# Optimization experiments

Hardware: AMD Instinct MI355X
Metric: run time of the kernel (lower is better)

The kernel has to match this reference:

```python
import jax, jax.numpy as jnp
import numpy as np

N = 32768
E = 524288
NFEAT = 256
NHID = 256
NUM_HEADS = 4
HEAD_DIM = NHID // NUM_HEADS
NLAYER = 2
EPS = 1e-5


def setup_inputs():
    keys = iter(jax.random.split(jax.random.key(0), 64))

    def nrm(shape, scale=0.05):
        return jax.random.normal(next(keys), shape, dtype=jnp.float32) * scale

    inp = {
        "x": jax.random.normal(next(keys), (N, NFEAT), dtype=jnp.float32),
        "edge_src": jax.random.randint(next(keys), (E,), 0, N),
        "edge_dst": jax.random.randint(next(keys), (E,), 0, N),
        "edge_attr": jax.random.uniform(next(keys), (E,), dtype=jnp.float32) * 0.1,
        "num_graphs": 64,
    }
    for i in range(NLAYER):
        fin = NFEAT if i == 0 else NHID
        inp["conv_w%d" % i] = nrm((fin, NHID))
        inp["bn_g%d" % i] = jnp.ones((NHID,), jnp.float32)
        inp["bn_b%d" % i] = jnp.zeros((NHID,), jnp.float32)
        inp["bn_m%d" % i] = nrm((NHID,), 0.1)
        inp["bn_v%d" % i] = 1.0 + jax.random.uniform(next(keys), (NHID,), dtype=jnp.float32) * 0.1
        inp["attn_in_w%d" % i] = nrm((3 * NHID, NHID))
        inp["attn_in_b%d" % i] = jnp.zeros((3 * NHID,), jnp.float32)
        inp["attn_out_w%d" % i] = nrm((NHID, NHID))
        inp["attn_out_b%d" % i] = jnp.zeros((NHID,), jnp.float32)
        inp["ln_g%d" % i] = jnp.ones((NHID,), jnp.float32)
        inp["ln_b%d" % i] = jnp.zeros((NHID,), jnp.float32)
    inp["score_w"] = nrm((1, NHID))
    inp["score_b"] = jnp.zeros((1,), jnp.float32)
    return inp


def _mha(xb, iw, ib, ow, ob):
    # torch.nn.MultiheadAttention (batch_first), all graphs same length so
    # key_padding_mask is all-False (no masked positions).
    B, S, H = xb.shape
    q, k, v = jnp.split(xb @ iw.T + ib, 3, axis=-1)
    heads = lambda t: t.reshape(B, S, NUM_HEADS, HEAD_DIM).transpose(0, 2, 1, 3)
    q, k, v = heads(q), heads(k), heads(v)
    scale = jnp.float32(1.0 / np.sqrt(HEAD_DIM))
    att = jax.nn.softmax(jnp.einsum("bhqd,bhkd->bhqk", q, k) * scale, axis=-1)
    o = jnp.einsum("bhqk,bhkd->bhqd", att, v).transpose(0, 2, 1, 3).reshape(B, S, H)
    return o @ ow.T + ob


def _forward(x, edge_attr, params, edge_src, edge_dst, num_graphs):
    n = x.shape[0]
    B = num_graphs
    S = n // B  # equal-sized graphs -> max_nodes == S, pad is a no-op
    h = x
    for i, (cw, bng, bnb, bnm, bnv, iw, ib, ow, ob, lg, lb) in enumerate(params):
        # DIGCNConv: out[dst] += edge_attr * (x @ W)[src]
        conv = jax.ops.segment_sum(edge_attr[:, None] * (h @ cw)[edge_src], edge_dst, num_segments=n)
        # BatchNorm1d (eval mode, running stats)
        conv = (conv - bnm) * jax.lax.rsqrt(bnv + EPS) * bng + bnb
        # ragged gather -> pad/stack -> MHA -> unpad (equal graph sizes => reshape)
        attended = _mha(conv.reshape(B, S, NHID), iw, ib, ow, ob).reshape(n, NHID)
        y = conv + attended
        mu = jnp.mean(y, axis=-1, keepdims=True)
        var = jnp.mean((y - mu) ** 2, axis=-1, keepdims=True)
        h = (y - mu) * jax.lax.rsqrt(var + EPS) * lg + lb  # LayerNorm
        if i < NLAYER - 1:
            h = jax.nn.relu(h)
    return h


def reference(x, edge_src, edge_dst, edge_attr, num_graphs,
              conv_w0, bn_g0, bn_b0, bn_m0, bn_v0, attn_in_w0, attn_in_b0, attn_out_w0, attn_out_b0, ln_g0, ln_b0,
              conv_w1, bn_g1, bn_b1, bn_m1, bn_v1, attn_in_w1, attn_in_b1, attn_out_w1, attn_out_b1, ln_g1, ln_b1,
              score_w, score_b):
    params = [
        (conv_w0, bn_g0, bn_b0, bn_m0, bn_v0, attn_in_w0, attn_in_b0, attn_out_w0, attn_out_b0, ln_g0, ln_b0),
        (conv_w1, bn_g1, bn_b1, bn_m1, bn_v1, attn_in_w1, attn_in_b1, attn_out_w1, attn_out_b1, ln_g1, ln_b1),
    ]
    h = _forward(x, edge_attr, params, edge_src, edge_dst, num_graphs)
    scores = (h @ score_w.T + score_b)[:, 0]
    # emb_list / score_list are per-graph views of these flat arrays
    return h, scores
```

## Files before the change

kernel.cpp:

```cpp
#include <hip/hip_runtime.h>
#include <hip/hip_bf16.h>
#include <math.h>

#define N_NODES 32768
#define E_EDGES 524288
#define NHID    256
#define HEAD_DIM 64
#define SEQ     512
#define EPS_LN  1e-5f
#define SM_SCALE 0.18033688011112042f

typedef __hip_bfloat16 bf16;
typedef __attribute__((ext_vector_type(8))) short short8;
typedef __attribute__((ext_vector_type(4))) float floatx4;
static const size_t NH = (size_t)N_NODES * NHID;

__device__ __forceinline__ void unpack2(unsigned int u, float& lo, float& hi) {
    union { float f; unsigned int i; } a, b;
    a.i = u << 16; b.i = u & 0xffff0000u;
    lo = a.f; hi = b.f;
}

__device__ __forceinline__ void* swzp(void* base, int row, int col) {
    return (char*)base + (((row << 7) + (col << 1)) ^ ((row & 7) << 4));
}

__device__ __forceinline__ void gload16(const bf16* g, void* lds) {
    __builtin_amdgcn_global_load_lds((const __attribute__((address_space(1))) void*)g,
                                     (__attribute__((address_space(3))) void*)lds, 16, 0, 0);
}

__global__ void k_cvtb4(bf16* __restrict__ dst, const float* __restrict__ src) {
    size_t i = (size_t)(blockIdx.x * 256 + threadIdx.x) * 4;
    const float4 v = *(const float4*)(src + i);
    __align__(8) bf16 tmp[4];
    tmp[0] = __float2bfloat16(v.x);
    tmp[1] = __float2bfloat16(v.y);
    tmp[2] = __float2bfloat16(v.z);
    tmp[3] = __float2bfloat16(v.w);
    *(uint2*)(dst + i) = *(uint2*)tmp;
}

__global__ __launch_bounds__(256) void k_stage(const float* __restrict__ cw,
                                               const float* __restrict__ bng,
                                               const float* __restrict__ bnb,
                                               const float* __restrict__ bnm,
                                               const float* __restrict__ bnv,
                                               const float* __restrict__ iw,
                                               const float* __restrict__ ow,
                                               bf16* __restrict__ iwb,
                                               bf16* __restrict__ owb,
                                               bf16* __restrict__ cwT,
                                               float* __restrict__ bns,
                                               float* __restrict__ bnt) {
    const int blk = blockIdx.x;
    const int tid = threadIdx.x;
    if (blk < 256) {
        const float* src = (blk < 192) ? iw : ow;
        bf16* dst = (blk < 192) ? iwb : owb;
        size_t i = (size_t)((blk < 192 ? blk : blk - 192) * 256 + tid) * 4;
        const float4 v = *(const float4*)(src + i);
        __align__(8) bf16 t4[4];
        t4[0] = __float2bfloat16(v.x);
        t4[1] = __float2bfloat16(v.y);
        t4[2] = __float2bfloat16(v.z);
        t4[3] = __float2bfloat16(v.w);
        *(uint2*)(dst + i) = *(uint2*)t4;
    } else if (blk < 512) {
        const int k = blk - 256;
        cwT[(size_t)tid * 256 + k] = __float2bfloat16(cw[(size_t)k * 256 + tid]);
    } else {
        float sv = bng[tid] * rsqrtf(bnv[tid] + EPS_LN);
        bns[tid] = sv;
        bnt[tid] = bnb[tid] - bnm[tid] * sv;
    }
}

__global__ void k_hist(const int* __restrict__ edst, int* __restrict__ counts) {
    int e = blockIdx.x * 256 + threadIdx.x;
    atomicAdd(&counts[edst[e]], 1);
}

__global__ __launch_bounds__(256) void k_scan(const int* __restrict__ counts,
                                              int* __restrict__ offsets,
                                              int* __restrict__ cursor) {
    __shared__ int sums[256];
    const int tid = threadIdx.x;
    const int base = tid * 128;
    int s = 0;
    for (int i = 0; i < 128; ++i) s += counts[base + i];
    sums[tid] = s;
    __syncthreads();
    for (int off = 1; off < 256; off <<= 1) {
        int v = (tid >= off) ? sums[tid - off] : 0;
        __syncthreads();
        sums[tid] += v;
        __syncthreads();
    }
    int run = (tid == 0) ? 0 : sums[tid - 1];
    for (int i = 0; i < 128; ++i) {
        int c = counts[base + i];
        offsets[base + i] = run;
        cursor[base + i] = run;
        run += c;
    }
    if (tid == 255) offsets[32768] = run;
}

__global__ void k_fill(const int* __restrict__ esrc, const int* __restrict__ edst,
                       const float* __restrict__ eattr, int* __restrict__ cursor,
                       int* __restrict__ srcp, float* __restrict__ attrp) {
    int e = blockIdx.x * 256 + threadIdx.x;
    int d = edst[e];
    int slot = atomicAdd(&cursor[d], 1);
    srcp[slot] = esrc[e];
    attrp[slot] = eattr[e];
}

__global__ __launch_bounds__(256) void k_gather(const bf16* __restrict__ t,
                                                const int* __restrict__ offsets,
                                                const int* __restrict__ srcp,
                                                const float* __restrict__ attrp,
                                                const float* __restrict__ bns,
                                                const float* __restrict__ bnt,
                                                bf16* __restrict__ conv) {
    const int node = (blockIdx.x * 256 + threadIdx.x) >> 6;
    const int lane = threadIdx.x & 63;
    const int half = lane >> 5;
    const int l32 = lane & 31;
    const int start = offsets[node];
    const int end = offsets[node + 1];
    float a[8];
#pragma unroll
    for (int i = 0; i < 8; ++i) a[i] = 0.f;
    for (int c0 = start; c0 < end; c0 += 64) {
        const int n = min(64, end - c0);
        int sidx = 0;
        float sa = 0.f;
        if (lane < n) {
            sidx = srcp[c0 + lane];
            sa = attrp[c0 + lane];
        }
        for (int j = 0; j < n; j += 2) {
            const int e = j + half;
            const int s = __shfl(sidx, e, 64);
            const float aw = __shfl(sa, e, 64);
            const uint4 u = *(const uint4*)(t + (size_t)s * 256 + l32 * 8);
            float v0, v1, v2, v3, v4, v5, v6, v7;
            unpack2(u.x, v0, v1);
            unpack2(u.y, v2, v3);
            unpack2(u.z, v4, v5);
            unpack2(u.w, v6, v7);
            a[0] = fmaf(aw, v0, a[0]);
            a[1] = fmaf(aw, v1, a[1]);
            a[2] = fmaf(aw, v2, a[2]);
            a[3] = fmaf(aw, v3, a[3]);
            a[4] = fmaf(aw, v4, a[4]);
            a[5] = fmaf(aw, v5, a[5]);
            a[6] = fmaf(aw, v6, a[6]);
            a[7] = fmaf(aw, v7, a[7]);
        }
    }
#pragma unroll
    for (int i = 0; i < 8; ++i) a[i] += __shfl_xor(a[i], 32, 64);
    if (half == 0) {
        const int c = l32 * 8;
        const float4 s0 = *(const float4*)(bns + c);
        const float4 s1 = *(const float4*)(bns + c + 4);
        const float4 t0 = *(const float4*)(bnt + c);
        const float4 t1 = *(const float4*)(bnt + c + 4);
        __align__(16) bf16 tmp[8];
        tmp[0] = __float2bfloat16(fmaf(a[0], s0.x, t0.x));
        tmp[1] = __float2bfloat16(fmaf(a[1], s0.y, t0.y));
        tmp[2] = __float2bfloat16(fmaf(a[2], s0.z, t0.z));
        tmp[3] = __float2bfloat16(fmaf(a[3], s0.w, t0.w));
        tmp[4] = __float2bfloat16(fmaf(a[4], s1.x, t1.x));
        tmp[5] = __float2bfloat16(fmaf(a[5], s1.y, t1.y));
        tmp[6] = __float2bfloat16(fmaf(a[6], s1.z, t1.z));
        tmp[7] = __float2bfloat16(fmaf(a[7], s1.w, t1.w));
        *(uint4*)(conv + (size_t)node * 256 + c) = *(uint4*)tmp;
    }
}

__global__ __launch_bounds__(256) void k_gemm(const bf16* __restrict__ A,
                                              const bf16* __restrict__ WT,
                                              const float* __restrict__ bias,
                                              bf16* __restrict__ C, bf16* __restrict__ VT,
                                              int ldc, int qkvmode) {
    __shared__ __align__(16) short As[2][128 * 64];
    __shared__ __align__(16) short Bs[2][128 * 64];
    const int tid = threadIdx.x;
    const int bm = blockIdx.x * 128;
    const int bn = blockIdx.y * 128;
    const int wid = tid >> 6;
    const int lane = tid & 63;
    const int wr = (wid >> 1) * 64;
    const int wc = (wid & 1) * 64;
    const int quad = lane >> 4;
    const int l16 = lane & 15;

    floatx4 acc[4][4];
#pragma unroll
    for (int mi = 0; mi < 4; ++mi)
#pragma unroll
        for (int ni = 0; ni < 4; ++ni)
            acc[mi][ni] = (floatx4){0.f, 0.f, 0.f, 0.f};

    auto STAGE = [&](int ks, int bf) {
#pragma unroll
        for (int t = 0; t < 4; ++t) {
            const int p = ((t * 4 + wid) << 10) + (lane << 4);
            const int row = p >> 7;
            const int cb = (p & 127) ^ ((row & 7) << 4);
            gload16(A + (size_t)(bm + row) * 256 + ks * 64 + (cb >> 1),
                    (char*)&As[bf][0] + ((t * 4 + wid) << 10));
            gload16(WT + (size_t)(bn + row) * 256 + ks * 64 + (cb >> 1),
                    (char*)&Bs[bf][0] + ((t * 4 + wid) << 10));
        }
    };

    STAGE(0, 0);
    __syncthreads();
    for (int t = 0; t < 4; ++t) {
        const int buf = t & 1;
        if (t < 3) STAGE(t + 1, buf ^ 1);
#pragma unroll
        for (int kk = 0; kk < 2; ++kk) {
            const int kcol = kk * 32 + quad * 8;
            short8 af[4], bfr[4];
#pragma unroll
            for (int mi = 0; mi < 4; ++mi)
                af[mi] = *(const short8*)swzp(&As[buf][0], wr + mi * 16 + l16, kcol);
#pragma unroll
            for (int ni = 0; ni < 4; ++ni)
                bfr[ni] = *(const short8*)swzp(&Bs[buf][0], wc + ni * 16 + l16, kcol);
#pragma unroll
            for (int mi = 0; mi < 4; ++mi)
#pragma unroll
                for (int ni = 0; ni < 4; ++ni)
                    acc[mi][ni] = __builtin_amdgcn_mfma_f32_16x16x32_bf16(af[mi], bfr[ni],
                                                                          acc[mi][ni], 0, 0, 0);
        }
        __syncthreads();
    }
    const float cs = (qkvmode && bn < 256) ? SM_SCALE : 1.0f;
    const bool vpath = (qkvmode && bn >= 512);
#pragma unroll
    for (int ni = 0; ni < 4; ++ni) {
        const int gc = bn + wc + ni * 16 + l16;
        const float bv = bias ? bias[gc] : 0.f;
#pragma unroll
        for (int mi = 0; mi < 4; ++mi) {
            const int gr = bm + wr + mi * 16 + quad * 4;
            if (vpath) {
                const int head = (gc - 512) >> 6;
                const int d = (gc - 512) & 63;
                const int bg = gr >> 9;
                const int sl = gr & 511;
                __align__(8) bf16 t4[4];
#pragma unroll
                for (int r = 0; r < 4; ++r) t4[r] = __float2bfloat16(acc[mi][ni][r] + bv);
                *(uint2*)(VT + (((size_t)((bg * 4 + head) * 64 + d)) << 9) + sl) = *(uint2*)t4;
            } else {
#pragma unroll
                for (int r = 0; r < 4; ++r)
                    C[(size_t)(gr + r) * ldc + gc] = __float2bfloat16((acc[mi][ni][r] + bv) * cs);
            }
        }
    }
}

__global__ __launch_bounds__(256) void k_fattn(const bf16* __restrict__ qkv,
                                               const bf16* __restrict__ vtb,
                                               bf16* __restrict__ ctx) {
    const int bid = ((blockIdx.x & 7) << 8) | (blockIdx.x >> 3);
    const int qt = bid & 7;
    const int head = (bid >> 3) & 3;
    const int b = bid >> 5;
    const int tid = threadIdx.x;
    const int wave = tid >> 6;
    const int lane = tid & 63;
    const int quad = lane >> 4;
    const int l16 = lane & 15;
    const int qrow0 = b * SEQ + qt * 64 + wave * 16;

    __shared__ __align__(16) short Ks[2][64 * 64];
    __shared__ __align__(16) short Vt[2][64 * 64];
    __shared__ __align__(16) short Ps[4][16 * 64];

    const bf16* kbase = qkv + (size_t)(b * SEQ) * 768 + 256 + head * HEAD_DIM;
    const bf16* vbase = vtb + (size_t)((b * 4 + head) * 64) * 512;
    const int pbase = (wave << 10) + (lane << 4);

    short8 af_q[2];
    {
        const bf16* qp = qkv + (size_t)(qrow0 + l16) * 768 + head * HEAD_DIM + quad * 8;
        af_q[0] = *(const short8*)(qp);
        af_q[1] = *(const short8*)(qp + 32);
    }
    short8 ones;
#pragma unroll
    for (int j = 0; j < 8; ++j) ones[j] = (short)0x3F80;

    floatx4 acc[5];
#pragma unroll
    for (int nt = 0; nt < 5; ++nt) acc[nt] = (floatx4){0.f, 0.f, 0.f, 0.f};

    auto STAGE = [&](int kt2, int bf) {
#pragma unroll
        for (int i = 0; i < 2; ++i) {
            const int p = (i << 12) + pbase;
            const int row = p >> 7;
            const int cb = (p & 127) ^ ((row & 7) << 4);
            gload16(kbase + (size_t)(kt2 * 64 + row) * 768 + (cb >> 1),
                    (char*)Ks[bf] + (i << 12) + (wave << 10));
            gload16(vbase + (size_t)row * 512 + kt2 * 64 + (cb >> 1),
                    (char*)Vt[bf] + (i << 12) + (wave << 10));
        }
    };

    STAGE(0, 0);
    __syncthreads();

    for (int kt = 0; kt < 8; ++kt) {
        const int buf = kt & 1;
        if (kt < 7) STAGE(kt + 1, buf ^ 1);

        floatx4 sf[4];
#pragma unroll
        for (int f = 0; f < 4; ++f) {
            const short8 bk0 = *(const short8*)swzp(Ks[buf], f * 16 + l16, quad * 8);
            const short8 bk1 = *(const short8*)swzp(Ks[buf], f * 16 + l16, 32 + quad * 8);
            sf[f] = __builtin_amdgcn_mfma_f32_16x16x32_bf16(af_q[0], bk0,
                                                            (floatx4){0.f, 0.f, 0.f, 0.f}, 0, 0, 0);
            sf[f] = __builtin_amdgcn_mfma_f32_16x16x32_bf16(af_q[1], bk1, sf[f], 0, 0, 0);
        }

        bf16* psb = (bf16*)&Ps[wave][0];
#pragma unroll
        for (int r = 0; r < 4; ++r) {
            const float p0 = exp2f(fminf(sf[0][r], 80.f));
            const float p1 = exp2f(fminf(sf[1][r], 80.f));
            const float p2 = exp2f(fminf(sf[2][r], 80.f));
            const float p3 = exp2f(fminf(sf[3][r], 80.f));
            const int qr = quad * 4 + r;
            *(bf16*)swzp(psb, qr, l16)      = __float2bfloat16(p0);
            *(bf16*)swzp(psb, qr, 16 + l16) = __float2bfloat16(p1);
            *(bf16*)swzp(psb, qr, 32 + l16) = __float2bfloat16(p2);
            *(bf16*)swzp(psb, qr, 48 + l16) = __float2bfloat16(p3);
        }

#pragma unroll
        for (int c2 = 0; c2 < 2; ++c2) {
            const short8 ap = *(const short8*)swzp(psb, l16, c2 * 32 + quad * 8);
#pragma unroll
            for (int nt = 0; nt < 4; ++nt) {
                const short8 bv = *(const short8*)swzp(Vt[buf], nt * 16 + l16, c2 * 32 + quad * 8);
                acc[nt] = __builtin_amdgcn_mfma_f32_16x16x32_bf16(ap, bv, acc[nt], 0, 0, 0);
            }
            acc[4] = __builtin_amdgcn_mfma_f32_16x16x32_bf16(ap, ones, acc[4], 0, 0, 0);
        }
        __syncthreads();
    }

#pragma unroll
    for (int r = 0; r < 4; ++r) {
        const float inv = 1.f / acc[4][r];
        bf16* op = ctx + (size_t)(qrow0 + quad * 4 + r) * 256 + head * HEAD_DIM + l16;
        op[0]  = __float2bfloat16(acc[0][r] * inv);
        op[16] = __float2bfloat16(acc[1][r] * inv);
        op[32] = __float2bfloat16(acc[2][r] * inv);
        op[48] = __float2bfloat16(acc[3][r] * inv);
    }
}

__global__ void k_ln(const bf16* __restrict__ conv, const bf16* __restrict__ proj,
                     const float* __restrict__ lg, const float* __restrict__ lb,
                     bf16* __restrict__ h) {
    int gt = blockIdx.x * blockDim.x + threadIdx.x;
    int node = gt >> 6;
    int lane = gt & 63;
    size_t base = (size_t)node * 256 + lane * 4;
    uint2 ua = *(const uint2*)(conv + base);
    uint2 up = *(const uint2*)(proj + base);
    float a0, a1, a2, a3, p0, p1, p2, p3;
    unpack2(ua.x, a0, a1);
    unpack2(ua.y, a2, a3);
    unpack2(up.x, p0, p1);
    unpack2(up.y, p2, p3);
    float y0 = a0 + p0, y1 = a1 + p1, y2 = a2 + p2, y3 = a3 + p3;
    float sum = y0 + y1 + y2 + y3;
#pragma unroll
    for (int off = 32; off > 0; off >>= 1) sum += __shfl_xor(sum, off, 64);
    float mu = sum * (1.0f / 256.0f);
    float d0 = y0 - mu, d1 = y1 - mu, d2 = y2 - mu, d3 = y3 - mu;
    float vs = d0 * d0 + d1 * d1 + d2 * d2 + d3 * d3;
#pragma unroll
    for (int off = 32; off > 0; off >>= 1) vs += __shfl_xor(vs, off, 64);
    float r = rsqrtf(vs * (1.0f / 256.0f) + EPS_LN);
    int c = lane * 4;
    float o0 = fmaxf(fmaf(d0 * r, lg[c + 0], lb[c + 0]), 0.f);
    float o1 = fmaxf(fmaf(d1 * r, lg[c + 1], lb[c + 1]), 0.f);
    float o2 = fmaxf(fmaf(d2 * r, lg[c + 2], lb[c + 2]), 0.f);
    float o3 = fmaxf(fmaf(d3 * r, lg[c + 3], lb[c + 3]), 0.f);
    __align__(8) bf16 tmp[4];
    tmp[0] = __float2bfloat16(o0);
    tmp[1] = __float2bfloat16(o1);
    tmp[2] = __float2bfloat16(o2);
    tmp[3] = __float2bfloat16(o3);
    *(uint2*)(h + base) = *(uint2*)tmp;
}

__global__ void k_lnout(const bf16* __restrict__ conv, const bf16* __restrict__ proj,
                        const float* __restrict__ lg, const float* __restrict__ lb,
                        const float* __restrict__ sw, const float* __restrict__ sb,
                        float* __restrict__ out) {
    int gt = blockIdx.x * blockDim.x + threadIdx.x;
    int node = gt >> 6;
    int lane = gt & 63;
    size_t base = (size_t)node * 256 + lane * 4;
    uint2 ua = *(const uint2*)(conv + base);
    uint2 up = *(const uint2*)(proj + base);
    float a0, a1, a2, a3, p0, p1, p2, p3;
    unpack2(ua.x, a0, a1);
    unpack2(ua.y, a2, a3);
    unpack2(up.x, p0, p1);
    unpack2(up.y, p2, p3);
    float y0 = a0 + p0, y1 = a1 + p1, y2 = a2 + p2, y3 = a3 + p3;
    float sum = y0 + y1 + y2 + y3;
#pragma unroll
    for (int off = 32; off > 0; off >>= 1) sum += __shfl_xor(sum, off, 64);
    float mu = sum * (1.0f / 256.0f);
    float d0 = y0 - mu, d1 = y1 - mu, d2 = y2 - mu, d3 = y3 - mu;
    float vs = d0 * d0 + d1 * d1 + d2 * d2 + d3 * d3;
#pragma unroll
    for (int off = 32; off > 0; off >>= 1) vs += __shfl_xor(vs, off, 64);
    float r = rsqrtf(vs * (1.0f / 256.0f) + EPS_LN);
    int c = lane * 4;
    float o0 = fmaf(d0 * r, lg[c + 0], lb[c + 0]);
    float o1 = fmaf(d1 * r, lg[c + 1], lb[c + 1]);
    float o2 = fmaf(d2 * r, lg[c + 2], lb[c + 2]);
    float o3 = fmaf(d3 * r, lg[c + 3], lb[c + 3]);
    *(float4*)(out + base) = make_float4(o0, o1, o2, o3);
    float part = o0 * sw[c + 0] + o1 * sw[c + 1] + o2 * sw[c + 2] + o3 * sw[c + 3];
#pragma unroll
    for (int off = 32; off > 0; off >>= 1) part += __shfl_xor(part, off, 64);
    if (lane == 0)
        out[(size_t)N_NODES * 256 + node] = part + sb[0];
}

extern "C" void kernel_launch(void* const* d_in, const int* in_sizes, int n_in,
                              void* d_out, int out_size, void* d_ws, size_t ws_size,
                              hipStream_t stream) {
    if (ws_size < (size_t)100663296) return;

    const float* x     = (const float*)d_in[0];
    const int*   esrc  = (const int*)d_in[1];
    const int*   edst  = (const int*)d_in[2];
    const float* eattr = (const float*)d_in[3];

    bf16* convb = (bf16*)d_ws;
    bf16* qkvb  = convb + NH;
    bf16* tb    = qkvb + 3 * NH;
    bf16* vtb   = tb + NH;
    bf16* xb  = qkvb;
    bf16* hb  = qkvb + NH;
    bf16* pjb = qkvb;

    char* scr = (char*)d_out;
    const size_t LBYTES = 393216 + 131072 + 131072 + 2048;
    int*   counts  = (int*)(scr + 2 * LBYTES);
    int*   offsets = counts + 32768;
    int*   cursor  = offsets + 32769;
    int*   srcp    = cursor + 32768;
    float* attrp   = (float*)(srcp + E_EDGES);

    (void)hipMemsetAsync(counts, 0, 32768 * sizeof(int), stream);
    k_hist<<<E_EDGES / 256, 256, 0, stream>>>(edst, counts);
    k_scan<<<1, 256, 0, stream>>>(counts, offsets, cursor);
    k_fill<<<E_EDGES / 256, 256, 0, stream>>>(esrc, edst, eattr, cursor, srcp, attrp);

    for (int L = 0; L < 2; ++L) {
        int bi = 5 + L * 11;
        char* base = scr + (size_t)L * LBYTES;
        bf16*  iwb = (bf16*)base;
        bf16*  owb = iwb + 196608;
        bf16*  cwT = owb + 65536;
        float* bns = (float*)(cwT + 65536);
        float* bnt = bns + 256;
        k_stage<<<513, 256, 0, stream>>>((const float*)d_in[bi + 0], (const float*)d_in[bi + 1],
                                         (const float*)d_in[bi + 2], (const float*)d_in[bi + 3],
                                         (const float*)d_in[bi + 4], (const float*)d_in[bi + 5],
                                         (const float*)d_in[bi + 7], iwb, owb, cwT, bns, bnt);
    }

    k_cvtb4<<<8192, 256, 0, stream>>>(xb, x);

    for (int L = 0; L < 2; ++L) {
        int bi = 5 + L * 11;
        char* base = scr + (size_t)L * LBYTES;
        bf16*  iwb = (bf16*)base;
        bf16*  owb = iwb + 196608;
        bf16*  cwT = owb + 65536;
        float* bns = (float*)(cwT + 65536);
        float* bnt = bns + 256;
        const float* ib = (const float*)d_in[bi + 6];
        const float* ob = (const float*)d_in[bi + 8];

        k_gemm<<<dim3(256, 2), 256, 0, stream>>>(L == 0 ? xb : hb, cwT, nullptr, tb, nullptr,
                                                 256, 0);
        k_gather<<<8192, 256, 0, stream>>>(tb, offsets, srcp, attrp, bns, bnt, convb);
        k_gemm<<<dim3(256, 6), 256, 0, stream>>>(convb, iwb, ib, qkvb, vtb, 768, 1);
        k_fattn<<<2048, 256, 0, stream>>>(qkvb, vtb, tb);
        k_gemm<<<dim3(256, 2), 256, 0, stream>>>(tb, owb, ob, pjb, nullptr, 256, 0);
        if (L == 0) {
            k_ln<<<8192, 256, 0, stream>>>(convb, pjb, (const float*)d_in[bi + 9],
                                           (const float*)d_in[bi + 10], hb);
        } else {
            k_lnout<<<8192, 256, 0, stream>>>(convb, pjb, (const float*)d_in[bi + 9],
                                              (const float*)d_in[bi + 10],
                                              (const float*)d_in[27], (const float*)d_in[28],
                                              (float*)d_out);
        }
    }
}
```

Measured before the change: 507.5 us.

## Fuse out-proj GEMM with LayerNorm/score, merge staging launches, prefetch gather rows

```diff
diff --git a/kernel.cpp b/kernel.cpp
--- a/kernel.cpp
+++ b/kernel.cpp
@@ -30,35 +30,49 @@
                                      (__attribute__((address_space(3))) void*)lds, 16, 0, 0);
 }
 
-__global__ void k_cvtb4(bf16* __restrict__ dst, const float* __restrict__ src) {
-    size_t i = (size_t)(blockIdx.x * 256 + threadIdx.x) * 4;
-    const float4 v = *(const float4*)(src + i);
-    __align__(8) bf16 tmp[4];
-    tmp[0] = __float2bfloat16(v.x);
-    tmp[1] = __float2bfloat16(v.y);
-    tmp[2] = __float2bfloat16(v.z);
-    tmp[3] = __float2bfloat16(v.w);
-    *(uint2*)(dst + i) = *(uint2*)tmp;
-}
-
-__global__ __launch_bounds__(256) void k_stage(const float* __restrict__ cw,
-                                               const float* __restrict__ bng,
-                                               const float* __restrict__ bnb,
-                                               const float* __restrict__ bnm,
-                                               const float* __restrict__ bnv,
-                                               const float* __restrict__ iw,
-                                               const float* __restrict__ ow,
-                                               bf16* __restrict__ iwb,
-                                               bf16* __restrict__ owb,
-                                               bf16* __restrict__ cwT,
-                                               float* __restrict__ bns,
-                                               float* __restrict__ bnt) {
+__global__ __launch_bounds__(256) void k_stage2(
+    const float* __restrict__ cw0, const float* __restrict__ g0, const float* __restrict__ b0,
+    const float* __restrict__ m0, const float* __restrict__ v0, const float* __restrict__ iw0,
+    const float* __restrict__ ow0,
+    const float* __restrict__ cw1, const float* __restrict__ g1, const float* __restrict__ b1,
+    const float* __restrict__ m1, const float* __restrict__ v1, const float* __restrict__ iw1,
+    const float* __restrict__ ow1,
+    bf16* __restrict__ iwb0, bf16* __restrict__ owb0, bf16* __restrict__ cwT0,
+    float* __restrict__ bns0, float* __restrict__ bnt0,
+    bf16* __restrict__ iwb1, bf16* __restrict__ owb1, bf16* __restrict__ cwT1,
+    float* __restrict__ bns1, float* __restrict__ bnt1,
+    const float* __restrict__ x, bf16* __restrict__ xb) {
     const int blk = blockIdx.x;
     const int tid = threadIdx.x;
-    if (blk < 256) {
-        const float* src = (blk < 192) ? iw : ow;
-        bf16* dst = (blk < 192) ? iwb : owb;
-        size_t i = (size_t)((blk < 192 ? blk : blk - 192) * 256 + tid) * 4;
+    if (blk >= 1026) {
+        size_t i = (size_t)((blk - 1026) * 256 + tid) * 4;
+        const float4 v = *(const float4*)(x + i);
+        __align__(8) bf16 t4[4];
+        t4[0] = __float2bfloat16(v.x);
+        t4[1] = __float2bfloat16(v.y);
+        t4[2] = __float2bfloat16(v.z);
+        t4[3] = __float2bfloat16(v.w);
+        *(uint2*)(xb + i) = *(uint2*)t4;
+        return;
+    }
+    const int L = (blk >= 513);
+    const int b2 = L ? blk - 513 : blk;
+    const float* cw = L ? cw1 : cw0;
+    const float* bng = L ? g1 : g0;
+    const float* bnb = L ? b1 : b0;
+    const float* bnm = L ? m1 : m0;
+    const float* bnv = L ? v1 : v0;
+    const float* iw = L ? iw1 : iw0;
+    const float* ow = L ? ow1 : ow0;
+    bf16* iwb = L ? iwb1 : iwb0;
+    bf16* owb = L ? owb1 : owb0;
+    bf16* cwT = L ? cwT1 : cwT0;
+    float* bns = L ? bns1 : bns0;
+    float* bnt = L ? bnt1 : bnt0;
+    if (b2 < 256) {
+        const float* src = (b2 < 192) ? iw : ow;
+        bf16* dst = (b2 < 192) ? iwb : owb;
+        size_t i = (size_t)((b2 < 192 ? b2 : b2 - 192) * 256 + tid) * 4;
         const float4 v = *(const float4*)(src + i);
         __align__(8) bf16 t4[4];
         t4[0] = __float2bfloat16(v.x);
@@ -66,8 +80,8 @@
         t4[2] = __float2bfloat16(v.z);
         t4[3] = __float2bfloat16(v.w);
         *(uint2*)(dst + i) = *(uint2*)t4;
-    } else if (blk < 512) {
-        const int k = blk - 256;
+    } else if (b2 < 512) {
+        const int k = b2 - 256;
         cwT[(size_t)tid * 256 + k] = __float2bfloat16(cw[(size_t)k * 256 + tid]);
     } else {
         float sv = bng[tid] * rsqrtf(bnv[tid] + EPS_LN);
@@ -141,11 +155,14 @@
             sidx = srcp[c0 + lane];
             sa = attrp[c0 + lane];
         }
+        int s = __shfl(sidx, half, 64);
+        float aw = __shfl(sa, half, 64);
+        uint4 u = *(const uint4*)(t + (size_t)s * 256 + l32 * 8);
         for (int j = 0; j < n; j += 2) {
-            const int e = j + half;
-            const int s = __shfl(sidx, e, 64);
-            const float aw = __shfl(sa, e, 64);
-            const uint4 u = *(const uint4*)(t + (size_t)s * 256 + l32 * 8);
+            const int e2 = (j + 2 + half) & 63;
+            const int s2 = __shfl(sidx, e2, 64);
+            const float aw2 = __shfl(sa, e2, 64);
+            const uint4 u2 = *(const uint4*)(t + (size_t)s2 * 256 + l32 * 8);
             float v0, v1, v2, v3, v4, v5, v6, v7;
             unpack2(u.x, v0, v1);
             unpack2(u.y, v2, v3);
@@ -159,6 +176,8 @@
             a[5] = fmaf(aw, v5, a[5]);
             a[6] = fmaf(aw, v6, a[6]);
             a[7] = fmaf(aw, v7, a[7]);
+            u = u2;
+            aw = aw2;
         }
     }
 #pragma unroll
@@ -270,6 +289,194 @@
     }
 }
 
+__global__ __launch_bounds__(256) void k_gemmln(const bf16* __restrict__ A,
+                                                const bf16* __restrict__ WT,
+                                                const float* __restrict__ bias,
+                                                const bf16* __restrict__ conv,
+                                                const float* __restrict__ lg,
+                                                const float* __restrict__ lb,
+                                                bf16* __restrict__ h,
+                                                const float* __restrict__ sw,
+                                                const float* __restrict__ sb,
+                                                float* __restrict__ out, int mode) {
+    __shared__ __align__(16) short As[2][64 * 64];
+    __shared__ __align__(16) short Bs[2][256 * 64];
+    const int tid = threadIdx.x;
+    const int bm = blockIdx.x * 64;
+    const int wid = tid >> 6;
+    const int lane = tid & 63;
+    const int wc = wid * 64;
+    const int quad = lane >> 4;
+    const int l16 = lane & 15;
+
+    floatx4 acc[4][4];
+#pragma unroll
+    for (int mi = 0; mi < 4; ++mi)
+#pragma unroll
+        for (int ni = 0; ni < 4; ++ni)
+            acc[mi][ni] = (floatx4){0.f, 0.f, 0.f, 0.f};
+
+    auto STAGE = [&](int ks, int bf) {
+#pragma unroll
+        for (int t = 0; t < 2; ++t) {
+            const int base = (t * 4 + wid) << 10;
+            const int p = base + (lane << 4);
+            const int row = p >> 7;
+            const int cb = (p & 127) ^ ((row & 7) << 4);
+            gload16(A + (size_t)(bm + row) * 256 + ks * 64 + (cb >> 1),
+                    (char*)&As[bf][0] + base);
+        }
+#pragma unroll
+        for (int t = 0; t < 8; ++t) {
+            const int base = (t * 4 + wid) << 10;
+            const int p = base + (lane << 4);
+            const int row = p >> 7;
+            const int cb = (p & 127) ^ ((row & 7) << 4);
+            gload16(WT + (size_t)row * 256 + ks * 64 + (cb >> 1), (char*)&Bs[bf][0] + base);
+        }
+    };
+
+    STAGE(0, 0);
+    __syncthreads();
+    for (int t = 0; t < 4; ++t) {
+        const int buf = t & 1;
+        if (t < 3) STAGE(t + 1, buf ^ 1);
+#pragma unroll
+        for (int kk = 0; kk < 2; ++kk) {
+            const int kcol = kk * 32 + quad * 8;
+            short8 af[4], bfr[4];
+#pragma unroll
+            for (int mi = 0; mi < 4; ++mi)
+                af[mi] = *(const short8*)swzp(&As[buf][0], mi * 16 + l16, kcol);
+#pragma unroll
+            for (int ni = 0; ni < 4; ++ni)
+                bfr[ni] = *(const short8*)swzp(&Bs[buf][0], wc + ni * 16 + l16, kcol);
+#pragma unroll
+            for (int mi = 0; mi < 4; ++mi)
+#pragma unroll
+                for (int ni = 0; ni < 4; ++ni)
+                    acc[mi][ni] = __builtin_amdgcn_mfma_f32_16x16x32_bf16(af[mi], bfr[ni],
+                                                                          acc[mi][ni], 0, 0, 0);
+        }
+        __syncthreads();
+    }
+
+#pragma unroll
+    for (int ni = 0; ni < 4; ++ni) {
+        const int gc = wc + ni * 16 + l16;
+        const float bv = bias[gc];
+#pragma unroll
+        for (int mi = 0; mi < 4; ++mi) {
+            const int gr = bm + mi * 16 + quad * 4;
+#pragma unroll
+            for (int r = 0; r < 4; ++r)
+                acc[mi][ni][r] += bv + __bfloat162float(conv[(size_t)(gr + r) * 256 + gc]);
+        }
+    }
+
+    float* red = (float*)&As[0][0];
+    float* red2 = red + 256;
+    float* red3 = red2 + 256;
+    float* redb = red3 + 256;
+
+#pragma unroll
+    for (int mi = 0; mi < 4; ++mi)
+#pragma unroll
+        for (int r = 0; r < 4; ++r) {
+            float s1 = acc[mi][0][r] + acc[mi][1][r] + acc[mi][2][r] + acc[mi][3][r];
+            s1 += __shfl_xor(s1, 1, 64);
+            s1 += __shfl_xor(s1, 2, 64);
+            s1 += __shfl_xor(s1, 4, 64);
+            s1 += __shfl_xor(s1, 8, 64);
+            if (l16 == 0) red[(mi * 16 + quad * 4 + r) * 4 + wid] = s1;
+        }
+    float lg4[4], lb4[4], w34[4];
+#pragma unroll
+    for (int ni = 0; ni < 4; ++ni) {
+        const int gc = wc + ni * 16 + l16;
+        lg4[ni] = lg[gc];
+        lb4[ni] = lb[gc];
+        w34[ni] = mode ? lg4[ni] * sw[gc] : 0.f;
+    }
+    if (mode) {
+        float pb = 0.f;
+#pragma unroll
+        for (int ni = 0; ni < 4; ++ni) pb += lb4[ni] * sw[wc + ni * 16 + l16];
+        pb += __shfl_xor(pb, 1, 64);
+        pb += __shfl_xor(pb, 2, 64);
+        pb += __shfl_xor(pb, 4, 64);
+        pb += __shfl_xor(pb, 8, 64);
+        if (lane == 0) redb[wid] = pb;
+    }
+    __syncthreads();
+
+    float mu_[4][4];
+#pragma unroll
+    for (int mi = 0; mi < 4; ++mi)
+#pragma unroll
+        for (int r = 0; r < 4; ++r) {
+            const int row = mi * 16 + quad * 4 + r;
+            const float mu = (red[row * 4 + 0] + red[row * 4 + 1] + red[row * 4 + 2] +
+                              red[row * 4 + 3]) * (1.f / 256.f);
+            mu_[mi][r] = mu;
+            float s2 = 0.f, s3 = 0.f;
+#pragma unroll
+            for (int ni = 0; ni < 4; ++ni) {
+                const float d = acc[mi][ni][r] - mu;
+                s2 += d * d;
+                s3 += d * w34[ni];
+            }
+            s2 += __shfl_xor(s2, 1, 64);
+            s2 += __shfl_xor(s2, 2, 64);
+            s2 += __shfl_xor(s2, 4, 64);
+            s2 += __shfl_xor(s2, 8, 64);
+            if (mode) {
+                s3 += __shfl_xor(s3, 1, 64);
+                s3 += __shfl_xor(s3, 2, 64);
+                s3 += __shfl_xor(s3, 4, 64);
+                s3 += __shfl_xor(s3, 8, 64);
+            }
+            if (l16 == 0) {
+                red2[row * 4 + wid] = s2;
+                if (mode) red3[row * 4 + wid] = s3;
+            }
+        }
+    __syncthreads();
+
+    const float B0 = mode ? (redb[0] + redb[1] + redb[2] + redb[3] + sb[0]) : 0.f;
+#pragma unroll
+    for (int mi = 0; mi < 4; ++mi)
+#pragma unroll
+        for (int r = 0; r < 4; ++r) {
+            const int row = mi * 16 + quad * 4 + r;
+            const int gr = bm + row;
+            const float mu = mu_[mi][r];
+            const float var = (red2[row * 4 + 0] + red2[row * 4 + 1] + red2[row * 4 + 2] +
+                               red2[row * 4 + 3]) * (1.f / 256.f);
+            const float rstd = rsqrtf(var + EPS_LN);
+            if (!mode) {
+#pragma unroll
+                for (int ni = 0; ni < 4; ++ni) {
+                    const int gc = wc + ni * 16 + l16;
+                    const float o = fmaf((acc[mi][ni][r] - mu) * rstd, lg4[ni], lb4[ni]);
+                    h[(size_t)gr * 256 + gc] = __float2bfloat16(fmaxf(o, 0.f));
+                }
+            } else {
+#pragma unroll
+                for (int ni = 0; ni < 4; ++ni) {
+                    const int gc = wc + ni * 16 + l16;
+                    out[(size_t)gr * 256 + gc] =
+                        fmaf((acc[mi][ni][r] - mu) * rstd, lg4[ni], lb4[ni]);
+                }
+                if (wid == 0 && l16 == 0) {
+                    const float S3 = red3[row * 4 + 0] + red3[row * 4 + 1] +
+                                     red3[row * 4 + 2] + red3[row * 4 + 3];
+                    out[(size_t)N_NODES * 256 + gr] = fmaf(rstd, S3, B0);
+                }
+            }
+        }
+}
+
 __global__ __launch_bounds__(256) void k_fattn(const bf16* __restrict__ qkv,
                                                const bf16* __restrict__ vtb,
                                                bf16* __restrict__ ctx) {
@@ -374,81 +581,6 @@
     }
 }
 
-__global__ void k_ln(const bf16* __restrict__ conv, const bf16* __restrict__ proj,
-                     const float* __restrict__ lg, const float* __restrict__ lb,
-                     bf16* __restrict__ h) {
-    int gt = blockIdx.x * blockDim.x + threadIdx.x;
-    int node = gt >> 6;
-    int lane = gt & 63;
-    size_t base = (size_t)node * 256 + lane * 4;
-    uint2 ua = *(const uint2*)(conv + base);
-    uint2 up = *(const uint2*)(proj + base);
-    float a0, a1, a2, a3, p0, p1, p2, p3;
-    unpack2(ua.x, a0, a1);
-    unpack2(ua.y, a2, a3);
-    unpack2(up.x, p0, p1);
-    unpack2(up.y, p2, p3);
-    float y0 = a0 + p0, y1 = a1 + p1, y2 = a2 + p2, y3 = a3 + p3;
-    float sum = y0 + y1 + y2 + y3;
-#pragma unroll
-    for (int off = 32; off > 0; off >>= 1) sum += __shfl_xor(sum, off, 64);
-    float mu = sum * (1.0f / 256.0f);
-    float d0 = y0 - mu, d1 = y1 - mu, d2 = y2 - mu, d3 = y3 - mu;
-    float vs = d0 * d0 + d1 * d1 + d2 * d2 + d3 * d3;
-#pragma unroll
-    for (int off = 32; off > 0; off >>= 1) vs += __shfl_xor(vs, off, 64);
-    float r = rsqrtf(vs * (1.0f / 256.0f) + EPS_LN);
-    int c = lane * 4;
-    float o0 = fmaxf(fmaf(d0 * r, lg[c + 0], lb[c + 0]), 0.f);
-    float o1 = fmaxf(fmaf(d1 * r, lg[c + 1], lb[c + 1]), 0.f);
-    float o2 = fmaxf(fmaf(d2 * r, lg[c + 2], lb[c + 2]), 0.f);
-    float o3 = fmaxf(fmaf(d3 * r, lg[c + 3], lb[c + 3]), 0.f);
-    __align__(8) bf16 tmp[4];
-    tmp[0] = __float2bfloat16(o0);
-    tmp[1] = __float2bfloat16(o1);
-    tmp[2] = __float2bfloat16(o2);
-    tmp[3] = __float2bfloat16(o3);
-    *(uint2*)(h + base) = *(uint2*)tmp;
-}
-
-__global__ void k_lnout(const bf16* __restrict__ conv, const bf16* __restrict__ proj,
-                        const float* __restrict__ lg, const float* __restrict__ lb,
-                        const float* __restrict__ sw, const float* __restrict__ sb,
-                        float* __restrict__ out) {
-    int gt = blockIdx.x * blockDim.x + threadIdx.x;
-    int node = gt >> 6;
-    int lane = gt & 63;
-    size_t base = (size_t)node * 256 + lane * 4;
-    uint2 ua = *(const uint2*)(conv + base);
-    uint2 up = *(const uint2*)(proj + base);
-    float a0, a1, a2, a3, p0, p1, p2, p3;
-    unpack2(ua.x, a0, a1);
-    unpack2(ua.y, a2, a3);
-    unpack2(up.x, p0, p1);
-    unpack2(up.y, p2, p3);
-    float y0 = a0 + p0, y1 = a1 + p1, y2 = a2 + p2, y3 = a3 + p3;
-    float sum = y0 + y1 + y2 + y3;
-#pragma unroll
-    for (int off = 32; off > 0; off >>= 1) sum += __shfl_xor(sum, off, 64);
-    float mu = sum * (1.0f / 256.0f);
-    float d0 = y0 - mu, d1 = y1 - mu, d2 = y2 - mu, d3 = y3 - mu;
-    float vs = d0 * d0 + d1 * d1 + d2 * d2 + d3 * d3;
-#pragma unroll
-    for (int off = 32; off > 0; off >>= 1) vs += __shfl_xor(vs, off, 64);
-    float r = rsqrtf(vs * (1.0f / 256.0f) + EPS_LN);
-    int c = lane * 4;
-    float o0 = fmaf(d0 * r, lg[c + 0], lb[c + 0]);
-    float o1 = fmaf(d1 * r, lg[c + 1], lb[c + 1]);
-    float o2 = fmaf(d2 * r, lg[c + 2], lb[c + 2]);
-    float o3 = fmaf(d3 * r, lg[c + 3], lb[c + 3]);
-    *(float4*)(out + base) = make_float4(o0, o1, o2, o3);
-    float part = o0 * sw[c + 0] + o1 * sw[c + 1] + o2 * sw[c + 2] + o3 * sw[c + 3];
-#pragma unroll
-    for (int off = 32; off > 0; off >>= 1) part += __shfl_xor(part, off, 64);
-    if (lane == 0)
-        out[(size_t)N_NODES * 256 + node] = part + sb[0];
-}
-
 extern "C" void kernel_launch(void* const* d_in, const int* in_sizes, int n_in,
                               void* d_out, int out_size, void* d_ws, size_t ws_size,
                               hipStream_t stream) {
@@ -465,7 +597,6 @@
     bf16* vtb   = tb + NH;
     bf16* xb  = qkvb;
     bf16* hb  = qkvb + NH;
-    bf16* pjb = qkvb;
 
     char* scr = (char*)d_out;
     const size_t LBYTES = 393216 + 131072 + 131072 + 2048;
@@ -480,47 +611,43 @@
     k_scan<<<1, 256, 0, stream>>>(counts, offsets, cursor);
     k_fill<<<E_EDGES / 256, 256, 0, stream>>>(esrc, edst, eattr, cursor, srcp, attrp);
 
+    bf16*  iwb[2];
+    bf16*  owb[2];
+    bf16*  cwT[2];
+    float* bns[2];
+    float* bnt[2];
+    for (int L = 0; L < 2; ++L) {
+        char* base = scr + (size_t)L * LBYTES;
+        iwb[L] = (bf16*)base;
+        owb[L] = iwb[L] + 196608;
+        cwT[L] = owb[L] + 65536;
+        bns[L] = (float*)(cwT[L] + 65536);
+        bnt[L] = bns[L] + 256;
+    }
+    k_stage2<<<9218, 256, 0, stream>>>(
+        (const float*)d_in[5], (const float*)d_in[6], (const float*)d_in[7],
+        (const float*)d_in[8], (const float*)d_in[9], (const float*)d_in[10],
+        (const float*)d_in[12],
+        (const float*)d_in[16], (const float*)d_in[17], (const float*)d_in[18],
+        (const float*)d_in[19], (const float*)d_in[20], (const float*)d_in[21],
+        (const float*)d_in[23],
+        iwb[0], owb[0], cwT[0], bns[0], bnt[0],
+        iwb[1], owb[1], cwT[1], bns[1], bnt[1],
+        x, xb);
+
     for (int L = 0; L < 2; ++L) {
         int bi = 5 + L * 11;
-        char* base = scr + (size_t)L * LBYTES;
-        bf16*  iwb = (bf16*)base;
-        bf16*  owb = iwb + 196608;
-        bf16*  cwT = owb + 65536;
-        float* bns = (float*)(cwT + 65536);
-        float* bnt = bns + 256;
-        k_stage<<<513, 256, 0, stream>>>((const float*)d_in[bi + 0], (const float*)d_in[bi + 1],
-                                         (const float*)d_in[bi + 2], (const float*)d_in[bi + 3],
-                                         (const float*)d_in[bi + 4], (const float*)d_in[bi + 5],
-                                         (const float*)d_in[bi + 7], iwb, owb, cwT, bns, bnt);
-    }
-
-    k_cvtb4<<<8192, 256, 0, stream>>>(xb, x);
-
-    for (int L = 0; L < 2; ++L) {
-        int bi = 5 + L * 11;
-        char* base = scr + (size_t)L * LBYTES;
-        bf16*  iwb = (bf16*)base;
-        bf16*  owb = iwb + 196608;
-        bf16*  cwT = owb + 65536;
-        float* bns = (float*)(cwT + 65536);
-        float* bnt = bns + 256;
         const float* ib = (const float*)d_in[bi + 6];
         const float* ob = (const float*)d_in[bi + 8];
 
-        k_gemm<<<dim3(256, 2), 256, 0, stream>>>(L == 0 ? xb : hb, cwT, nullptr, tb, nullptr,
-                                                 256, 0);
-        k_gather<<<8192, 256, 0, stream>>>(tb, offsets, srcp, attrp, bns, bnt, convb);
-        k_gemm<<<dim3(256, 6), 256, 0, stream>>>(convb, iwb, ib, qkvb, vtb, 768, 1);
+        k_gemm<<<dim3(256, 2), 256, 0, stream>>>(L == 0 ? xb : hb, cwT[L], nullptr, tb,
+                                                 nullptr, 256, 0);
+        k_gather<<<8192, 256, 0, stream>>>(tb, offsets, srcp, attrp, bns[L], bnt[L], convb);
+        k_gemm<<<dim3(256, 6), 256, 0, stream>>>(convb, iwb[L], ib, qkvb, vtb, 768, 1);
         k_fattn<<<2048, 256, 0, stream>>>(qkvb, vtb, tb);
-        k_gemm<<<dim3(256, 2), 256, 0, stream>>>(tb, owb, ob, pjb, nullptr, 256, 0);
-        if (L == 0) {
-            k_ln<<<8192, 256, 0, stream>>>(convb, pjb, (const float*)d_in[bi + 9],
-                                           (const float*)d_in[bi + 10], hb);
-        } else {
-            k_lnout<<<8192, 256, 0, stream>>>(convb, pjb, (const float*)d_in[bi + 9],
-                                              (const float*)d_in[bi + 10],
-                                              (const float*)d_in[27], (const float*)d_in[28],
-                                              (float*)d_out);
-        }
-    }
-}
+        k_gemmln<<<512, 256, 0, stream>>>(tb, owb[L], ob, convb, (const float*)d_in[bi + 9],
+                                          (const float*)d_in[bi + 10], hb,
+                                          (const float*)d_in[27], (const float*)d_in[28],
+                                          (float*)d_out, L);
+    }
+}
```

After: 495.3 us. 2.4% less time.
